# Optimization experiments

Measured on AMD Instinct MI355X. Metric: run time of the kernel, lower is better.

## Reference

```python
import jax, jax.numpy as jnp
import numpy as np

B, S, DIM = 2, 2048, 2048
H, KVH, HD = 16, 4, 128
G = H // KVH  # GQA groups = 4
THETA = 10000.0


def setup_inputs() -> dict:
    key = jax.random.key(0)
    k0, k1, k2, k3, k4 = jax.random.split(key, 5)
    x = jax.random.normal(k0, (B, S, DIM), jnp.float32)
    # RoPE table: [max_seq_len, head_dim//2, 2] holding (cos, sin)
    inv_freq = 1.0 / (THETA ** (jnp.arange(0, HD, 2, dtype=jnp.float32) / HD))
    angles = jnp.outer(jnp.arange(S, dtype=jnp.float32), inv_freq)  # [S, HD//2]
    freqs_cis = jnp.stack([jnp.cos(angles), jnp.sin(angles)], axis=-1)
    sc = 0.02
    wq = jax.random.normal(k1, (H * HD, DIM), jnp.float32) * sc
    wk = jax.random.normal(k2, (KVH * HD, DIM), jnp.float32) * sc
    wv = jax.random.normal(k3, (KVH * HD, DIM), jnp.float32) * sc
    wo = jax.random.normal(k4, (DIM, H * HD), jnp.float32) * sc
    return {"x": x, "freqs_cis": freqs_cis, "wq": wq, "wk": wk, "wv": wv, "wo": wo}


def apply_rope(x, freqs_cis):
    # x: [B, S, h, HD]; freqs_cis: [max_S, HD//2, 2]
    s = x.shape[1]
    xr = x.astype(jnp.float32).reshape(*x.shape[:-1], -1, 2)  # [B,S,h,HD//2,2]
    cos = freqs_cis[:s, :, 0][None, :, None, :]  # [1,S,1,HD//2]
    sin = freqs_cis[:s, :, 1][None, :, None, :]
    x0, x1 = xr[..., 0], xr[..., 1]
    out = jnp.stack([x0 * cos - x1 * sin, x0 * sin + x1 * cos], axis=-1)
    return out.reshape(x.shape).astype(x.dtype)


def reference(x, freqs_cis, wq, wk, wv, wo):
    b, s, d = x.shape
    q = (x @ wq.T).reshape(b, s, H, HD)
    k = (x @ wk.T).reshape(b, s, KVH, HD)
    v = (x @ wv.T).reshape(b, s, KVH, HD)
    q = apply_rope(q, freqs_cis)
    k = apply_rope(k, freqs_cis)
    # GQA expand: repeat_interleave along head dim
    k = jnp.repeat(k, G, axis=2)  # [b,s,H,HD]
    v = jnp.repeat(v, G, axis=2)
    q = jnp.swapaxes(q, 1, 2)  # [b,H,s,HD]
    k = jnp.swapaxes(k, 1, 2)
    v = jnp.swapaxes(v, 1, 2)
    scale = 1.0 / jnp.sqrt(jnp.asarray(HD, dtype=q.dtype))
    scores = jnp.einsum('bhqd,bhkd->bhqk', q, k) * scale  # [b,H,s,s]
    causal = jnp.tril(jnp.ones((s, s), dtype=bool))
    scores = jnp.where(causal[None, None], scores, jnp.finfo(scores.dtype).min)
    probs = jax.nn.softmax(scores, axis=-1)
    attn = jnp.einsum('bhqk,bhkd->bhqd', probs, v)  # [b,H,s,HD]
    attn = jnp.swapaxes(attn, 1, 2).reshape(b, s, H * HD)
    return attn @ wo.T
```

## Files before the change

### kernel.cpp

```cpp
#include <hip/hip_runtime.h>
#include <stdint.h>

#define B_ 2
#define S_ 2048
#define DIM_ 2048
#define H_ 16
#define KVH_ 4
#define HD_ 128

typedef short short8 __attribute__((ext_vector_type(8)));
typedef float f4 __attribute__((ext_vector_type(4)));
typedef float f16v __attribute__((ext_vector_type(16)));
typedef unsigned int uint2v __attribute__((ext_vector_type(2)));
typedef unsigned short u16;

#define KSCALE (0.08838834764831845f * 1.4426950408889634f)

__device__ __forceinline__ float bf2f(u16 u) {
    union { unsigned int i; float f; } c; c.i = ((unsigned int)u) << 16; return c.f;
}
__device__ __forceinline__ u16 f2bf(float f) {
    union { float f; unsigned int i; } c; c.f = f;
    return (u16)((c.i + 0x7fffu + ((c.i >> 16) & 1u)) >> 16);
}
__device__ __forceinline__ unsigned pk_bf16(float lo, float hi) {
    unsigned r;
    asm("v_cvt_pk_bf16_f32 %0, %1, %2" : "=v"(r) : "v"(lo), "v"(hi));
    return r;
}

#define GLDS16(gp, lp) \
    __builtin_amdgcn_global_load_lds((const __attribute__((address_space(1))) unsigned int*)(gp), \
                                     (__attribute__((address_space(3))) unsigned int*)(lp), 16, 0, 0)

#define BAR()     asm volatile("s_barrier" ::: "memory")
#define WAITLGKM() asm volatile("s_waitcnt lgkmcnt(0)" ::: "memory")

__global__ void cast_all(const float* __restrict__ x,  const float* __restrict__ wq,
                         const float* __restrict__ wk, const float* __restrict__ wv,
                         const float* __restrict__ wo,
                         u16* __restrict__ xb, u16* __restrict__ wqkvb, u16* __restrict__ wob) {
    int i = blockIdx.x * 256 + threadIdx.x;
    const float4* src; ushort4* dst; int j;
    if (i < 2097152)      { src = (const float4*)x;  dst = (ushort4*)xb;                 j = i; }
    else if (i < 3145728) { src = (const float4*)wq; dst = (ushort4*)wqkvb;              j = i - 2097152; }
    else if (i < 3407872) { src = (const float4*)wk; dst = (ushort4*)wqkvb + 1048576;    j = i - 3145728; }
    else if (i < 3670016) { src = (const float4*)wv; dst = (ushort4*)wqkvb + 1310720;    j = i - 3407872; }
    else                  { src = (const float4*)wo; dst = (ushort4*)wob;                j = i - 3670016; }
    float4 v = src[j];
    ushort4 o;
    o.x = f2bf(v.x); o.y = f2bf(v.y); o.z = f2bf(v.z); o.w = f2bf(v.w);
    dst[j] = o;
}

template<bool OUT_BF16, int NBX>
__global__ __launch_bounds__(512, 2) void gemm256(const u16* __restrict__ A,
                                                  const u16* __restrict__ W,
                                                  void* __restrict__ Cout,
                                                  int M, int N, int K) {
    __shared__ u16 As[2][16384];
    __shared__ u16 Bs[2][16384];
    int t = threadIdx.x, lane = t & 63, w = t >> 6;
    int quad = lane >> 4, l16 = lane & 15, l7 = lane & 7;
    int wm = w >> 2, wn = w & 3;
    int bid = blockIdx.x;
    int xcd = bid & 7, grp = bid >> 3;
    int bx = grp % NBX, by = (grp / NBX) * 8 + xcd;
    size_t m0 = (size_t)by * 256, n0 = (size_t)bx * 256;

    int srow = lane >> 3;
    int sunit = (lane & 7) ^ srow;
    int rR0a = (w >> 2) * 64 + (w & 3) * 8;
    const u16* Ag = A + (m0 + srow) * (size_t)K + sunit * 8;
    const u16* Bg = W + (n0 + srow) * (size_t)K + sunit * 8;

#define STG_A(pl, tk, r0) GLDS16(Ag + ((size_t)((r0) + w * 8)) * K + (tk) * 64, (pl) + ((r0) + w * 8) * 64)
#define STG_B(pl, tk, r0) GLDS16(Bg + ((size_t)((r0) + w * 8)) * K + (tk) * 64, (pl) + ((r0) + w * 8) * 64)
#define STG_BR(pl, tk, bse) GLDS16(Bg + ((size_t)((bse) + rR0a)) * K + (tk) * 64, (pl) + ((bse) + rR0a) * 64)

#define LDA(mh) { \
    _Pragma("unroll") for (int i_ = 0; i_ < 4; i_++) \
    _Pragma("unroll") for (int k_ = 0; k_ < 2; k_++) \
        a[i_][k_] = *(const short8*)&pAc[(wm * 128 + (mh) * 64 + i_ * 16 + l16) * 64 + (((quad + 4 * k_) ^ l7) << 3)]; }
#define LDB(nh) { \
    _Pragma("unroll") for (int j_ = 0; j_ < 2; j_++) \
    _Pragma("unroll") for (int k_ = 0; k_ < 2; k_++) \
        b[j_][k_] = *(const short8*)&pBc[(wn * 64 + (nh) * 32 + j_ * 16 + l16) * 64 + (((quad + 4 * k_) ^ l7) << 3)]; }
#define MFMA_Q(mh, nh) { \
    __builtin_amdgcn_s_setprio(1); \
    _Pragma("unroll") for (int i_ = 0; i_ < 4; i_++) \
    _Pragma("unroll") for (int j_ = 0; j_ < 2; j_++) \
    _Pragma("unroll") for (int k_ = 0; k_ < 2; k_++) \
        acc[(mh) * 4 + i_][(nh) * 2 + j_] = __builtin_amdgcn_mfma_f32_16x16x32_bf16( \
            a[i_][k_], b[j_][k_], acc[(mh) * 4 + i_][(nh) * 2 + j_], 0, 0, 0); \
    __builtin_amdgcn_s_setprio(0); }

    f4 acc[8][4];
    #pragma unroll
    for (int i = 0; i < 8; i++)
        #pragma unroll
        for (int j = 0; j < 4; j++) acc[i][j] = (f4){0.f, 0.f, 0.f, 0.f};

    int NT = K >> 6;

    #pragma unroll
    for (int pt = 0; pt < 2; pt++) {
        u16* pa = &As[pt][0]; u16* pb = &Bs[pt][0];
        #pragma unroll
        for (int r0 = 0; r0 < 256; r0 += 64) { STG_A(pa, pt, r0); STG_B(pb, pt, r0); }
    }
    asm volatile("s_waitcnt vmcnt(0)" ::: "memory");
    BAR();

    short8 a[4][2], b[2][2];
    for (int tt = 0; tt < NT; tt++) {
        int c = tt & 1, nc = c ^ 1;
        u16* pAc = &As[c][0];  u16* pBc = &Bs[c][0];
        u16* pAn = &As[nc][0]; u16* pBn = &Bs[nc][0];
        bool s1 = (tt >= 1) & (tt + 1 < NT);
        bool s2 = (tt + 2 < NT);
        LDA(0); LDB(0);
        if (s1) { STG_A(pAn, tt + 1, 64); STG_A(pAn, tt + 1, 192); }
        BAR(); WAITLGKM(); MFMA_Q(0, 0); BAR();
        LDB(1);
        if (s1) { STG_BR(pBn, tt + 1, 32); STG_BR(pBn, tt + 1, 160); }
        BAR(); WAITLGKM(); MFMA_Q(0, 1); BAR();
        LDA(1); LDB(0);
        if (s2) { STG_A(pAc, tt + 2, 0); STG_A(pAc, tt + 2, 128); }
        BAR(); WAITLGKM(); MFMA_Q(1, 0); BAR();
        if (s2) asm volatile("s_waitcnt vmcnt(2)" ::: "memory");
        else    asm volatile("s_waitcnt vmcnt(0)" ::: "memory");
        LDB(1);
        if (s2) { STG_BR(pBc, tt + 2, 0); STG_BR(pBc, tt + 2, 128); }
        BAR(); WAITLGKM(); MFMA_Q(1, 1); BAR();
    }

    #pragma unroll
    for (int i = 0; i < 8; i++) {
        size_t row = m0 + wm * 128 + i * 16 + quad * 4;
        #pragma unroll
        for (int j = 0; j < 4; j++) {
            size_t col = n0 + wn * 64 + j * 16 + l16;
            #pragma unroll
            for (int r = 0; r < 4; r++) {
                if (OUT_BF16) ((u16*)Cout)[(row + r) * (size_t)N + col] = f2bf(acc[i][j][r]);
                else          ((float*)Cout)[(row + r) * (size_t)N + col] = acc[i][j][r];
            }
        }
    }
#undef STG_A
#undef STG_B
#undef STG_BR
#undef LDA
#undef LDB
#undef MFMA_Q
}

__global__ __launch_bounds__(256) void pack_k(const u16* __restrict__ QKV,
                                              const float* __restrict__ freqs,
                                              u16* __restrict__ Kp) {
    int gid = blockIdx.x * 256 + threadIdx.x;
    int lane = gid & 63, j = (gid >> 6) & 1, ds = (gid >> 7) & 7;
    int kt = (gid >> 10) & 31, bk = gid >> 15;
    int b = bk >> 2, kvh = bk & 3;
    int l31 = lane & 31, hi = lane >> 5;
    int s = kt * 64 + j * 32 + l31;
    int d0 = ds * 16 + hi * 8;
    const u16* src = QKV + (size_t)(b * S_ + s) * 3072 + 2048 + kvh * HD_ + d0;
    short8 v = *(const short8*)src;
    short8 o;
    #pragma unroll
    for (int jp = 0; jp < 4; jp++) {
        float2 cw = ((const float2*)freqs)[s * 64 + ds * 8 + hi * 4 + jp];
        float x0 = bf2f((u16)v[2 * jp]), x1 = bf2f((u16)v[2 * jp + 1]);
        o[2 * jp]     = (short)f2bf(x0 * cw.x - x1 * cw.y);
        o[2 * jp + 1] = (short)f2bf(x0 * cw.y + x1 * cw.x);
    }
    *(short8*)&Kp[(size_t)gid * 8] = o;
}

__global__ __launch_bounds__(256) void pack_v(const u16* __restrict__ QKV, u16* __restrict__ Vp) {
    __shared__ u16 L[64 * 136];
    int bid = blockIdx.x;
    int bk = bid & 7, kt = bid >> 3;
    int b = bk >> 2, kvh = bk & 3;
    int t = threadIdx.x;
    const u16* src = QKV + (size_t)(b * S_ + kt * 64) * 3072 + 2560 + kvh * HD_;
    #pragma unroll
    for (int it = 0; it < 4; it++) {
        int idx = t + it * 256;
        int r = idx >> 4, c = idx & 15;
        *(short8*)&L[r * 136 + c * 8] = *(const short8*)(src + (size_t)r * 3072 + c * 8);
    }
    __syncthreads();
    u16* dst = Vp + (size_t)(bk * 32 + kt) * 8192;
    #pragma unroll
    for (int it = 0; it < 4; it++) {
        int idx = t + it * 256;
        int frag = idx >> 6, lane = idx & 63;
        int ks = frag >> 2, ht = frag & 3;
        int hd = ht * 32 + (lane & 31);
        int k0 = ks * 16 + (lane >> 5) * 8;
        short8 v;
        #pragma unroll
        for (int jj = 0; jj < 8; jj++) v[jj] = (short)L[(k0 + jj) * 136 + hd];
        *(short8*)&dst[(size_t)idx * 8] = v;
    }
}

__global__ __launch_bounds__(64, 2)
void attn_kernel(const u16* __restrict__ QKV,
                 const float* __restrict__ freqs,
                 const u16* __restrict__ Kp,
                 const u16* __restrict__ Vp,
                 u16* __restrict__ Ob) {
    int bid = blockIdx.x;
    int k8 = bid >> 8;
    int c  = bid & 255;
    int bk = c & 7, h4 = (c >> 3) & 3, tq = c >> 5;
    int qb = k8 * 8 + ((k8 & 1) ? 7 - tq : tq);
    int b = bk >> 2, kvh = bk & 3;
    int lane = threadIdx.x;
    int l31 = lane & 31, hi = lane >> 5;
    int h = kvh * 4 + h4;
    int nkt = (qb >> 1) + 1;

    short8 qf[8];
    {
        int s = qb * 32 + l31;
        const u16* qp = QKV + ((size_t)(b * S_ + s)) * 3072 + h * HD_ + hi * 8;
        const float2* fr2 = (const float2*)freqs;
        #pragma unroll
        for (int ds = 0; ds < 8; ds++) {
            short8 v = *(const short8*)(qp + ds * 16);
            short8 o;
            #pragma unroll
            for (int jp = 0; jp < 4; jp++) {
                float2 cs = fr2[s * 64 + ds * 8 + hi * 4 + jp];
                float x0 = bf2f((u16)v[2 * jp]), x1 = bf2f((u16)v[2 * jp + 1]);
                o[2 * jp]     = (short)f2bf((x0 * cs.x - x1 * cs.y) * KSCALE);
                o[2 * jp + 1] = (short)f2bf((x0 * cs.y + x1 * cs.x) * KSCALE);
            }
            qf[ds] = o;
        }
    }

    float m_i = -3e38f, ls = 0.f;
    f16v o4[4];
    #pragma unroll
    for (int i = 0; i < 4; i++)
        #pragma unroll
        for (int r = 0; r < 16; r++) o4[i][r] = 0.f;

    const u16* Kpb = Kp + (size_t)bk * 32 * 8192;
    const u16* Vpb = Vp + (size_t)bk * 32 * 8192;

    for (int kt = 0; kt < nkt; kt++) {
        const u16* kb = Kpb + (size_t)kt * 8192 + lane * 8;
        const u16* vb = Vpb + (size_t)kt * 8192 + lane * 8;

        f16v sacc[2];
        #pragma unroll
        for (int k2 = 0; k2 < 2; k2++)
            #pragma unroll
            for (int r = 0; r < 16; r++) sacc[k2][r] = 0.f;
        #pragma unroll
        for (int ds = 0; ds < 8; ds++) {
            short8 kf0 = *(const short8*)(kb + ds * 1024);
            short8 kf1 = *(const short8*)(kb + ds * 1024 + 512);
            sacc[0] = __builtin_amdgcn_mfma_f32_32x32x16_bf16(kf0, qf[ds], sacc[0], 0, 0, 0);
            sacc[1] = __builtin_amdgcn_mfma_f32_32x32x16_bf16(kf1, qf[ds], sacc[1], 0, 0, 0);
        }

        short8 vf[16];
        #pragma unroll
        for (int f = 0; f < 16; f++) vf[f] = *(const short8*)(vb + f * 512);

        if (kt == nkt - 1) {
            int off0 = kt * 64 - qb * 32;
            #pragma unroll
            for (int k2 = 0; k2 < 2; k2++) {
                #pragma unroll
                for (int r = 0; r < 16; r++) {
                    int colo = off0 + k2 * 32 + (r & 3) + ((r >> 2) << 3) + (hi << 2);
                    if (colo > l31) sacc[k2][r] = -3e38f;
                }
            }
        }

        float mx[16];
        #pragma unroll
        for (int r = 0; r < 16; r++) mx[r] = fmaxf(sacc[0][r], sacc[1][r]);
        #pragma unroll
        for (int s_ = 8; s_ > 0; s_ >>= 1)
            #pragma unroll
            for (int r = 0; r < s_; r++) mx[r] = fmaxf(mx[r], mx[r + s_]);
        float pm = fmaxf(mx[0], __shfl_xor(mx[0], 32, 64));
        if (__any(pm > m_i + 8.0f)) {
            float mnew = fmaxf(m_i, pm);
            float al = exp2f(m_i - mnew);
            ls *= al;
            #pragma unroll
            for (int i = 0; i < 4; i++)
                #pragma unroll
                for (int r = 0; r < 16; r++) o4[i][r] *= al;
            m_i = mnew;
        }

        short8 pa[4];
        #pragma unroll
        for (int k2 = 0; k2 < 2; k2++) {
            float p[16];
            #pragma unroll
            for (int r = 0; r < 16; r++) p[r] = exp2f(sacc[k2][r] - m_i);
            float s0 = (p[0] + p[1]) + (p[2] + p[3]);
            float s1 = (p[4] + p[5]) + (p[6] + p[7]);
            float s2 = (p[8] + p[9]) + (p[10] + p[11]);
            float s3 = (p[12] + p[13]) + (p[14] + p[15]);
            ls += (s0 + s1) + (s2 + s3);
            unsigned W0 = pk_bf16(p[0], p[1]),   W1 = pk_bf16(p[2], p[3]);
            unsigned W2 = pk_bf16(p[4], p[5]),   W3 = pk_bf16(p[6], p[7]);
            unsigned W4 = pk_bf16(p[8], p[9]),   W5 = pk_bf16(p[10], p[11]);
            unsigned W6 = pk_bf16(p[12], p[13]), W7 = pk_bf16(p[14], p[15]);
            uint2v r02 = __builtin_amdgcn_permlane32_swap(W0, W2, false, false);
            uint2v r13 = __builtin_amdgcn_permlane32_swap(W1, W3, false, false);
            uint2v r46 = __builtin_amdgcn_permlane32_swap(W4, W6, false, false);
            uint2v r57 = __builtin_amdgcn_permlane32_swap(W5, W7, false, false);
            union { unsigned u[4]; short8 s8; } flo, fhi;
            flo.u[0] = r02[0]; flo.u[1] = r13[0]; flo.u[2] = r02[1]; flo.u[3] = r13[1];
            fhi.u[0] = r46[0]; fhi.u[1] = r57[0]; fhi.u[2] = r46[1]; fhi.u[3] = r57[1];
            pa[k2 * 2]     = flo.s8;
            pa[k2 * 2 + 1] = fhi.s8;
        }

        __builtin_amdgcn_s_setprio(1);
        #pragma unroll
        for (int ks = 0; ks < 4; ks++) {
            #pragma unroll
            for (int ht = 0; ht < 4; ht++)
                o4[ht] = __builtin_amdgcn_mfma_f32_32x32x16_bf16(vf[ks * 4 + ht], pa[ks], o4[ht], 0, 0, 0);
        }
        __builtin_amdgcn_s_setprio(0);
    }

    ls += __shfl_xor(ls, 32, 64);
    float rl = 1.0f / ls;
    size_t row = (size_t)b * S_ + qb * 32 + l31;
    u16* op = Ob + row * 2048 + h * HD_;
    #pragma unroll
    for (int ht = 0; ht < 4; ht++) {
        #pragma unroll
        for (int g = 0; g < 4; g++) {
            ushort4 st;
            st.x = f2bf(o4[ht][4 * g + 0] * rl);
            st.y = f2bf(o4[ht][4 * g + 1] * rl);
            st.z = f2bf(o4[ht][4 * g + 2] * rl);
            st.w = f2bf(o4[ht][4 * g + 3] * rl);
            *(ushort4*)&op[ht * 32 + g * 8 + hi * 4] = st;
        }
    }
}

extern "C" void kernel_launch(void* const* d_in, const int* in_sizes, int n_in,
                              void* d_out, int out_size, void* d_ws, size_t ws_size,
                              hipStream_t stream) {
    const float* x     = (const float*)d_in[0];
    const float* freqs = (const float*)d_in[1];
    const float* wq    = (const float*)d_in[2];
    const float* wk    = (const float*)d_in[3];
    const float* wv    = (const float*)d_in[4];
    const float* wo    = (const float*)d_in[5];
    float* out = (float*)d_out;

    char* p = (char*)d_ws;
    u16* xb    = (u16*)p; p += (size_t)4096 * 2048 * 2;
    u16* wqkvb = (u16*)p; p += (size_t)3072 * 2048 * 2;
    u16* wob   = (u16*)p; p += (size_t)2048 * 2048 * 2;
    u16* QKVb  = (u16*)p; p += (size_t)4096 * 3072 * 2;
    u16* Kpb   = (u16*)p; p += (size_t)8 * 32 * 8192 * 2;
    u16* Vpb   = (u16*)p; p += (size_t)8 * 32 * 8192 * 2;
    u16* attnb = xb;

    cast_all<<<18432, 256, 0, stream>>>(x, wq, wk, wv, wo, xb, wqkvb, wob);

    gemm256<true, 12><<<192, 512, 0, stream>>>(xb, wqkvb, QKVb, 4096, 3072, 2048);

    pack_k<<<1024, 256, 0, stream>>>(QKVb, freqs, Kpb);
    pack_v<<<256, 256, 0, stream>>>(QKVb, Vpb);

    attn_kernel<<<2048, 64, 0, stream>>>(QKVb, freqs, Kpb, Vpb, attnb);

    gemm256<false, 8><<<128, 512, 0, stream>>>(attnb, wob, out, 4096, 2048, 2048);
}
```

Baseline: 319.9 us.

## Prefetch next K tile into registers and split QK accumulation chains

```diff
diff --git a/kernel.cpp b/kernel.cpp
--- a/kernel.cpp
+++ b/kernel.cpp
@@ -35,6 +35,7 @@
 
 #define BAR()     asm volatile("s_barrier" ::: "memory")
 #define WAITLGKM() asm volatile("s_waitcnt lgkmcnt(0)" ::: "memory")
+#define SCHEDB()  __builtin_amdgcn_sched_barrier(0)
 
 __global__ void cast_all(const float* __restrict__ x,  const float* __restrict__ wq,
                          const float* __restrict__ wk, const float* __restrict__ wv,
@@ -208,7 +209,7 @@
     }
 }
 
-__global__ __launch_bounds__(64, 2)
+__global__ __launch_bounds__(64, 1)
 void attn_kernel(const u16* __restrict__ QKV,
                  const float* __restrict__ freqs,
                  const u16* __restrict__ Kp,
@@ -218,7 +219,7 @@
     int k8 = bid >> 8;
     int c  = bid & 255;
     int bk = c & 7, h4 = (c >> 3) & 3, tq = c >> 5;
-    int qb = k8 * 8 + ((k8 & 1) ? 7 - tq : tq);
+    int qb = 63 - (k8 * 8 + ((k8 & 1) ? 7 - tq : tq));
     int b = bk >> 2, kvh = bk & 3;
     int lane = threadIdx.x;
     int l31 = lane & 31, hi = lane >> 5;
@@ -252,29 +253,50 @@
         #pragma unroll
         for (int r = 0; r < 16; r++) o4[i][r] = 0.f;
 
-    const u16* Kpb = Kp + (size_t)bk * 32 * 8192;
-    const u16* Vpb = Vp + (size_t)bk * 32 * 8192;
+    const u16* Kpb = Kp + (size_t)bk * 32 * 8192 + lane * 8;
+    const u16* Vpb = Vp + (size_t)bk * 32 * 8192 + lane * 8;
+
+    short8 kf[16];
+    #pragma unroll
+    for (int f = 0; f < 16; f++) kf[f] = *(const short8*)(Kpb + f * 512);
 
     for (int kt = 0; kt < nkt; kt++) {
-        const u16* kb = Kpb + (size_t)kt * 8192 + lane * 8;
-        const u16* vb = Vpb + (size_t)kt * 8192 + lane * 8;
+        short8 vf[16];
+        {
+            const u16* vb = Vpb + (size_t)kt * 8192;
+            #pragma unroll
+            for (int f = 0; f < 16; f++) vf[f] = *(const short8*)(vb + f * 512);
+        }
+        SCHEDB();
+
+        f16v sA[2], sB[2];
+        #pragma unroll
+        for (int k2 = 0; k2 < 2; k2++)
+            #pragma unroll
+            for (int r = 0; r < 16; r++) { sA[k2][r] = 0.f; sB[k2][r] = 0.f; }
+        __builtin_amdgcn_s_setprio(1);
+        #pragma unroll
+        for (int ds = 0; ds < 4; ds++) {
+            sA[0] = __builtin_amdgcn_mfma_f32_32x32x16_bf16(kf[ds * 2],     qf[ds], sA[0], 0, 0, 0);
+            sA[1] = __builtin_amdgcn_mfma_f32_32x32x16_bf16(kf[ds * 2 + 1], qf[ds], sA[1], 0, 0, 0);
+            sB[0] = __builtin_amdgcn_mfma_f32_32x32x16_bf16(kf[(ds + 4) * 2],     qf[ds + 4], sB[0], 0, 0, 0);
+            sB[1] = __builtin_amdgcn_mfma_f32_32x32x16_bf16(kf[(ds + 4) * 2 + 1], qf[ds + 4], sB[1], 0, 0, 0);
+        }
+        __builtin_amdgcn_s_setprio(0);
+        SCHEDB();
+
+        if (kt + 1 < nkt) {
+            const u16* kb = Kpb + (size_t)(kt + 1) * 8192;
+            #pragma unroll
+            for (int f = 0; f < 16; f++) kf[f] = *(const short8*)(kb + f * 512);
+        }
+        SCHEDB();
 
         f16v sacc[2];
         #pragma unroll
         for (int k2 = 0; k2 < 2; k2++)
             #pragma unroll
-            for (int r = 0; r < 16; r++) sacc[k2][r] = 0.f;
-        #pragma unroll
-        for (int ds = 0; ds < 8; ds++) {
-            short8 kf0 = *(const short8*)(kb + ds * 1024);
-            short8 kf1 = *(const short8*)(kb + ds * 1024 + 512);
-            sacc[0] = __builtin_amdgcn_mfma_f32_32x32x16_bf16(kf0, qf[ds], sacc[0], 0, 0, 0);
-            sacc[1] = __builtin_amdgcn_mfma_f32_32x32x16_bf16(kf1, qf[ds], sacc[1], 0, 0, 0);
-        }
-
-        short8 vf[16];
-        #pragma unroll
-        for (int f = 0; f < 16; f++) vf[f] = *(const short8*)(vb + f * 512);
+            for (int r = 0; r < 16; r++) sacc[k2][r] = sA[k2][r] + sB[k2][r];
 
         if (kt == nkt - 1) {
             int off0 = kt * 64 - qb * 32;
@@ -332,6 +354,7 @@
             pa[k2 * 2]     = flo.s8;
             pa[k2 * 2 + 1] = fhi.s8;
         }
+        SCHEDB();
 
         __builtin_amdgcn_s_setprio(1);
         #pragma unroll
```

After: 318.0 us. Within noise of the previous version (-0.6%).

## Split long causal attention rows across two blocks and combine partials

Applied to the files above, without the earlier changes.

```diff
diff --git a/kernel.cpp b/kernel.cpp
--- a/kernel.cpp
+++ b/kernel.cpp
@@ -208,22 +208,30 @@
     }
 }
 
-__global__ __launch_bounds__(64, 2)
+__global__ __launch_bounds__(64, 3)
 void attn_kernel(const u16* __restrict__ QKV,
                  const float* __restrict__ freqs,
                  const u16* __restrict__ Kp,
                  const u16* __restrict__ Vp,
-                 u16* __restrict__ Ob) {
+                 u16* __restrict__ Ob,
+                 float* __restrict__ Po,
+                 float* __restrict__ Pm,
+                 int split_ok) {
     int bid = blockIdx.x;
-    int k8 = bid >> 8;
-    int c  = bid & 255;
-    int bk = c & 7, h4 = (c >> 3) & 3, tq = c >> 5;
-    int qb = k8 * 8 + ((k8 & 1) ? 7 - tq : tq);
+    int qb = 63 - (bid >> 6);
+    int c2 = bid & 63;
+    int bk = c2 & 7, h4 = (c2 >> 3) & 3, chunk = (c2 >> 5) & 1;
+    int nkt = (qb >> 1) + 1;
+    int split = split_ok && (qb >= 32);
+    if (!split && chunk) return;
+    int nh = (nkt + 1) >> 1;
+    int kt0 = (split && chunk) ? nh : 0;
+    int kt1 = split ? (chunk ? nkt : nh) : nkt;
+
     int b = bk >> 2, kvh = bk & 3;
     int lane = threadIdx.x;
     int l31 = lane & 31, hi = lane >> 5;
     int h = kvh * 4 + h4;
-    int nkt = (qb >> 1) + 1;
 
     short8 qf[8];
     {
@@ -252,18 +260,19 @@
         #pragma unroll
         for (int r = 0; r < 16; r++) o4[i][r] = 0.f;
 
-    const u16* Kpb = Kp + (size_t)bk * 32 * 8192;
-    const u16* Vpb = Vp + (size_t)bk * 32 * 8192;
-
-    for (int kt = 0; kt < nkt; kt++) {
-        const u16* kb = Kpb + (size_t)kt * 8192 + lane * 8;
-        const u16* vb = Vpb + (size_t)kt * 8192 + lane * 8;
+    const u16* Kpb = Kp + (size_t)bk * 32 * 8192 + lane * 8;
+    const u16* Vpb = Vp + (size_t)bk * 32 * 8192 + lane * 8;
+
+    for (int kt = kt0; kt < kt1; kt++) {
+        const u16* kb = Kpb + (size_t)kt * 8192;
+        const u16* vb = Vpb + (size_t)kt * 8192;
 
         f16v sacc[2];
         #pragma unroll
         for (int k2 = 0; k2 < 2; k2++)
             #pragma unroll
             for (int r = 0; r < 16; r++) sacc[k2][r] = 0.f;
+        __builtin_amdgcn_s_setprio(1);
         #pragma unroll
         for (int ds = 0; ds < 8; ds++) {
             short8 kf0 = *(const short8*)(kb + ds * 1024);
@@ -271,10 +280,7 @@
             sacc[0] = __builtin_amdgcn_mfma_f32_32x32x16_bf16(kf0, qf[ds], sacc[0], 0, 0, 0);
             sacc[1] = __builtin_amdgcn_mfma_f32_32x32x16_bf16(kf1, qf[ds], sacc[1], 0, 0, 0);
         }
-
-        short8 vf[16];
-        #pragma unroll
-        for (int f = 0; f < 16; f++) vf[f] = *(const short8*)(vb + f * 512);
+        __builtin_amdgcn_s_setprio(0);
 
         if (kt == nkt - 1) {
             int off0 = kt * 64 - qb * 32;
@@ -337,25 +343,73 @@
         #pragma unroll
         for (int ks = 0; ks < 4; ks++) {
             #pragma unroll
-            for (int ht = 0; ht < 4; ht++)
-                o4[ht] = __builtin_amdgcn_mfma_f32_32x32x16_bf16(vf[ks * 4 + ht], pa[ks], o4[ht], 0, 0, 0);
+            for (int ht = 0; ht < 4; ht++) {
+                short8 vf = *(const short8*)(vb + (ks * 4 + ht) * 512);
+                o4[ht] = __builtin_amdgcn_mfma_f32_32x32x16_bf16(vf, pa[ks], o4[ht], 0, 0, 0);
+            }
         }
         __builtin_amdgcn_s_setprio(0);
     }
 
     ls += __shfl_xor(ls, 32, 64);
-    float rl = 1.0f / ls;
+    if (split) {
+        int slot = ((bk * 4 + h4) * 32 + (qb - 32)) * 2 + chunk;
+        float* po = Po + (size_t)slot * 4096 + lane * 64;
+        #pragma unroll
+        for (int ht = 0; ht < 4; ht++)
+            #pragma unroll
+            for (int r = 0; r < 16; r++) po[ht * 16 + r] = o4[ht][r];
+        Pm[(size_t)slot * 128 + lane * 2]     = m_i;
+        Pm[(size_t)slot * 128 + lane * 2 + 1] = ls;
+    } else {
+        float rl = 1.0f / ls;
+        size_t row = (size_t)b * S_ + qb * 32 + l31;
+        u16* op = Ob + row * 2048 + h * HD_;
+        #pragma unroll
+        for (int ht = 0; ht < 4; ht++) {
+            #pragma unroll
+            for (int g = 0; g < 4; g++) {
+                ushort4 st;
+                st.x = f2bf(o4[ht][4 * g + 0] * rl);
+                st.y = f2bf(o4[ht][4 * g + 1] * rl);
+                st.z = f2bf(o4[ht][4 * g + 2] * rl);
+                st.w = f2bf(o4[ht][4 * g + 3] * rl);
+                *(ushort4*)&op[ht * 32 + g * 8 + hi * 4] = st;
+            }
+        }
+    }
+}
+
+__global__ __launch_bounds__(64) void attn_combine(const float* __restrict__ Po,
+                                                   const float* __restrict__ Pm,
+                                                   u16* __restrict__ Ob) {
+    int cid = blockIdx.x;
+    int bk = cid & 7, h4 = (cid >> 3) & 3, qq = cid >> 5;
+    int qb = 32 + qq;
+    int b = bk >> 2, kvh = bk & 3;
+    int h = kvh * 4 + h4;
+    int lane = threadIdx.x;
+    int l31 = lane & 31, hi = lane >> 5;
+    int s0 = ((bk * 4 + h4) * 32 + qq) * 2;
+    float m0 = Pm[(size_t)s0 * 128 + lane * 2],       l0 = Pm[(size_t)s0 * 128 + lane * 2 + 1];
+    float m1 = Pm[(size_t)(s0 + 1) * 128 + lane * 2], l1 = Pm[(size_t)(s0 + 1) * 128 + lane * 2 + 1];
+    float M  = fmaxf(m0, m1);
+    float a0 = exp2f(m0 - M), a1 = exp2f(m1 - M);
+    float rl = 1.0f / (l0 * a0 + l1 * a1);
+    const float4* q0 = (const float4*)(Po + (size_t)s0 * 4096 + lane * 64);
+    const float4* q1 = (const float4*)(Po + (size_t)(s0 + 1) * 4096 + lane * 64);
     size_t row = (size_t)b * S_ + qb * 32 + l31;
     u16* op = Ob + row * 2048 + h * HD_;
     #pragma unroll
     for (int ht = 0; ht < 4; ht++) {
         #pragma unroll
         for (int g = 0; g < 4; g++) {
+            float4 v0 = q0[ht * 4 + g], v1 = q1[ht * 4 + g];
             ushort4 st;
-            st.x = f2bf(o4[ht][4 * g + 0] * rl);
-            st.y = f2bf(o4[ht][4 * g + 1] * rl);
-            st.z = f2bf(o4[ht][4 * g + 2] * rl);
-            st.w = f2bf(o4[ht][4 * g + 3] * rl);
+            st.x = f2bf((v0.x * a0 + v1.x * a1) * rl);
+            st.y = f2bf((v0.y * a0 + v1.y * a1) * rl);
+            st.z = f2bf((v0.z * a0 + v1.z * a1) * rl);
+            st.w = f2bf((v0.w * a0 + v1.w * a1) * rl);
             *(ushort4*)&op[ht * 32 + g * 8 + hi * 4] = st;
         }
     }
@@ -379,7 +433,12 @@
     u16* QKVb  = (u16*)p; p += (size_t)4096 * 3072 * 2;
     u16* Kpb   = (u16*)p; p += (size_t)8 * 32 * 8192 * 2;
     u16* Vpb   = (u16*)p; p += (size_t)8 * 32 * 8192 * 2;
+    float* Po  = (float*)p; p += (size_t)2048 * 4096 * 4;
+    float* Pm  = (float*)p; p += (size_t)2048 * 128 * 4;
     u16* attnb = xb;
+
+    size_t need = (size_t)(p - (char*)d_ws);
+    int split_ok = (ws_size >= need) ? 1 : 0;
 
     cast_all<<<18432, 256, 0, stream>>>(x, wq, wk, wv, wo, xb, wqkvb, wob);
 
@@ -388,7 +447,8 @@
     pack_k<<<1024, 256, 0, stream>>>(QKVb, freqs, Kpb);
     pack_v<<<256, 256, 0, stream>>>(QKVb, Vpb);
 
-    attn_kernel<<<2048, 64, 0, stream>>>(QKVb, freqs, Kpb, Vpb, attnb);
+    attn_kernel<<<4096, 64, 0, stream>>>(QKVb, freqs, Kpb, Vpb, attnb, Po, Pm, split_ok);
+    if (split_ok) attn_combine<<<1024, 64, 0, stream>>>(Po, Pm, attnb);
 
     gemm256<false, 8><<<128, 512, 0, stream>>>(attnb, wob, out, 4096, 2048, 2048);
 }
```

New measurement: 364.0 us. 1.14x slower.
